# Kernel optimization log

Measured on AMD Instinct MI355X. Metric: run time of the kernel, lower is better.

Reference implementation:

```python
import jax, jax.numpy as jnp
import numpy as np

B, S, D, H = 2, 2048, 1024, 16
HD = D // H  # head size 64

def setup_inputs() -> dict:
    key = jax.random.key(0)
    ks = jax.random.split(key, 7)
    sc = 1.0 / np.sqrt(D)
    return {
        "batch_data": jax.random.normal(ks[0], (B, S, D), dtype=jnp.float32),
        "Wq": jax.random.normal(ks[1], (D, D), dtype=jnp.float32) * sc,
        "bq": jnp.zeros((D,), dtype=jnp.float32),
        "Wk": jax.random.normal(ks[2], (D, D), dtype=jnp.float32) * sc,
        "bk": jnp.zeros((D,), dtype=jnp.float32),
        "Wv": jax.random.normal(ks[3], (D, D), dtype=jnp.float32) * sc,
        "bv": jnp.zeros((D,), dtype=jnp.float32),
    }

def _split_heads(x):
    # [B,S,D] -> [B,H,S,HD]
    b, s, _ = x.shape
    return x.reshape(b, s, H, HD).transpose(0, 2, 1, 3)

def reference(batch_data, Wq, bq, Wk, bk, Wv, bv):
    q = _split_heads(batch_data @ Wq + bq)
    k = _split_heads(batch_data @ Wk + bk)
    v = _split_heads(batch_data @ Wv + bv)
    scores = jnp.einsum('bhqd,bhkd->bhqk', q, k) / jnp.sqrt(jnp.float32(HD))
    probs = jax.nn.softmax(scores, axis=-1)
    ctx = jnp.einsum('bhqk,bhkd->bhqd', probs, v)  # [B,H,S,HD]
    ctx = ctx.transpose(0, 2, 1, 3).reshape(batch_data.shape[0], batch_data.shape[1], D)
    return jnp.mean(ctx, axis=1)  # mean pool over sequence -> [B,D]
```

## Files before the change

### kernel.cpp

```cpp
#include <hip/hip_runtime.h>
#include <hip/hip_bf16.h>
#include <stdint.h>

#define B_  2
#define S_  2048
#define D_  1024
#define H_  16
#define HD_ 64

typedef __attribute__((ext_vector_type(8)))  __bf16 bf16x8;
typedef __attribute__((ext_vector_type(4)))  __bf16 bf16x4;
typedef __attribute__((ext_vector_type(2)))  __bf16 bf16x2;
typedef __attribute__((ext_vector_type(4)))  short  s16x4;
typedef __attribute__((ext_vector_type(4)))  float  f32x4;
typedef __attribute__((ext_vector_type(16))) float  f32x16;
typedef __attribute__((ext_vector_type(2)))  uint32_t u32x2;
typedef __attribute__((ext_vector_type(4)))  uint32_t u32x4;

#define QSCALE 0.18033688011112042f

#if __has_builtin(__builtin_amdgcn_mfma_f32_32x32x8bf16_1k)
#define HAVE_MFMA_K8 1
#else
#define HAVE_MFMA_K8 0
#endif

__device__ __forceinline__ void gload16(const void* g, void* l) {
  __builtin_amdgcn_global_load_lds(
      (__attribute__((address_space(1))) void*)(uintptr_t)g,
      (__attribute__((address_space(3))) void*)(uintptr_t)l,
      16, 0, 0);
}

__global__ __launch_bounds__(256) void prep(
    const float* __restrict__ x, const float* __restrict__ wq,
    const float* __restrict__ wk, const float* __restrict__ wv,
    __bf16* __restrict__ xb, __bf16* __restrict__ wt, float* __restrict__ out) {
  __shared__ float tile[32][33];
  const int t = threadIdx.x;
  const int bx = blockIdx.x;
  if (bx < 4096) {
    int i = bx * 256 + t;
    float4 v = ((const float4*)x)[i];
    bf16x4 o;
    o[0] = (__bf16)v.x; o[1] = (__bf16)v.y; o[2] = (__bf16)v.z; o[3] = (__bf16)v.w;
    ((bf16x4*)xb)[i] = o;
  } else if (bx < 7168) {
    int tb = bx - 4096;
    int z = tb >> 10;
    int rem = tb & 1023;
    int n0 = (rem & 31) * 32, k0 = (rem >> 5) * 32;
    const float* w = (z == 0) ? wq : (z == 1 ? wk : wv);
    __bf16* o = wt + (size_t)z * D_ * D_;
    int tx = t & 31, ty = t >> 5;
    for (int i = 0; i < 4; ++i)
      tile[ty + 8 * i][tx] = w[(size_t)(k0 + ty + 8 * i) * D_ + n0 + tx];
    __syncthreads();
    for (int i = 0; i < 4; ++i)
      o[(size_t)(n0 + ty + 8 * i) * D_ + k0 + tx] = (__bf16)tile[tx][ty + 8 * i];
  } else {
    float4* o4 = (float4*)out;
    float4 z4 = {0.f, 0.f, 0.f, 0.f};
    o4[t] = z4;
    o4[t + 256] = z4;
  }
}

__global__ __launch_bounds__(256, 3) void gemm_qkv(
    const __bf16* __restrict__ xb, const __bf16* __restrict__ wt,
    const float* __restrict__ bq, const float* __restrict__ bk,
    const float* __restrict__ bv, __bf16* __restrict__ qh,
    __bf16* __restrict__ kh, __bf16* __restrict__ vt) {
  constexpr int K = 1024;
  constexpr int NIT = K / 32;
  __shared__ __attribute__((aligned(16))) __bf16 lA[2][128 * 32];
  __shared__ __attribute__((aligned(16))) __bf16 lB[2][128 * 32];

  const int z = blockIdx.z;
  const __bf16* w = wt + (size_t)z * K * D_;
  const float* bias = (z == 0) ? bq : (z == 1 ? bk : bv);
  const int t = threadIdx.x;
  const int lane = t & 63;
  const int wid = t >> 6;
  const int quad = lane >> 4;
  const int col = lane & 15;
  const int m0 = blockIdx.x * 128;
  const int n0 = blockIdx.y * 128;
  const int wr = (wid >> 1) * 64;
  const int wc = (wid & 1) * 64;

  const int sr0 = t >> 2;
  const int gc = (t & 3) ^ ((t >> 2) & 3);

  auto stage = [&](int kt, int buf) {
    gload16(xb + (size_t)(m0 + sr0) * K + kt * 32 + gc * 8,
            (char*)&lA[buf][0] + t * 16);
    gload16(xb + (size_t)(m0 + 64 + sr0) * K + kt * 32 + gc * 8,
            (char*)&lA[buf][0] + 4096 + t * 16);
    gload16(w + (size_t)(n0 + sr0) * K + kt * 32 + gc * 8,
            (char*)&lB[buf][0] + t * 16);
    gload16(w + (size_t)(n0 + 64 + sr0) * K + kt * 32 + gc * 8,
            (char*)&lB[buf][0] + 4096 + t * 16);
  };

  f32x4 acc[4][4] = {};

  stage(0, 0);

  if (z < 2) {
    for (int kt = 0; kt < NIT; ++kt) {
      const int cur = kt & 1;
      __syncthreads();
      if (kt + 1 < NIT) stage(kt + 1, cur ^ 1);
      bf16x8 fw[4], fx[4];
      for (int i = 0; i < 4; ++i) {
        int n = wr + i * 16 + col;
        int sl = quad ^ (n & 3);
        fw[i] = *(const bf16x8*)((const char*)&lB[cur][0] + n * 64 + sl * 16);
      }
      for (int j = 0; j < 4; ++j) {
        int m = wc + j * 16 + col;
        int sl = quad ^ (m & 3);
        fx[j] = *(const bf16x8*)((const char*)&lA[cur][0] + m * 64 + sl * 16);
      }
      for (int i = 0; i < 4; ++i)
        for (int j = 0; j < 4; ++j)
          acc[i][j] = __builtin_amdgcn_mfma_f32_16x16x32_bf16(
              fw[i], fx[j], acc[i][j], 0, 0, 0);
    }
    const float scale = (z == 0) ? QSCALE : 1.0f;
    __bf16* dst = (z == 0) ? qh : kh;
    for (int i = 0; i < 4; ++i) {
      int gnb = n0 + wr + i * 16 + quad * 4;
      float4 bi = *(const float4*)(bias + gnb);
      int h = gnb >> 6, hd = gnb & 63;
      for (int j = 0; j < 4; ++j) {
        int gm = m0 + wc + j * 16 + col;
        int b = gm >> 11, s = gm & 2047;
        bf16x4 pk;
        pk[0] = (__bf16)((acc[i][j][0] + bi.x) * scale);
        pk[1] = (__bf16)((acc[i][j][1] + bi.y) * scale);
        pk[2] = (__bf16)((acc[i][j][2] + bi.z) * scale);
        pk[3] = (__bf16)((acc[i][j][3] + bi.w) * scale);
        *(bf16x4*)(dst + ((size_t)(b * H_ + h) * S_ + s) * HD_ + hd) = pk;
      }
    }
  } else {
    for (int kt = 0; kt < NIT; ++kt) {
      const int cur = kt & 1;
      __syncthreads();
      if (kt + 1 < NIT) stage(kt + 1, cur ^ 1);
      bf16x8 fx[4], fw[4];
      for (int i = 0; i < 4; ++i) {
        int m = wr + i * 16 + col;
        int sl = quad ^ (m & 3);
        fx[i] = *(const bf16x8*)((const char*)&lA[cur][0] + m * 64 + sl * 16);
      }
      for (int j = 0; j < 4; ++j) {
        int n = wc + j * 16 + col;
        int sl = quad ^ (n & 3);
        fw[j] = *(const bf16x8*)((const char*)&lB[cur][0] + n * 64 + sl * 16);
      }
      for (int i = 0; i < 4; ++i)
        for (int j = 0; j < 4; ++j)
          acc[i][j] = __builtin_amdgcn_mfma_f32_16x16x32_bf16(
              fx[i], fw[j], acc[i][j], 0, 0, 0);
    }
    for (int i = 0; i < 4; ++i) {
      int gmb = m0 + wr + i * 16 + quad * 4;
      int b = gmb >> 11, s = gmb & 2047;
      for (int j = 0; j < 4; ++j) {
        int gn = n0 + wc + j * 16 + col;
        int h = gn >> 6, hd = gn & 63;
        float bi = bias[gn];
        bf16x4 pk;
        pk[0] = (__bf16)(acc[i][j][0] + bi);
        pk[1] = (__bf16)(acc[i][j][1] + bi);
        pk[2] = (__bf16)(acc[i][j][2] + bi);
        pk[3] = (__bf16)(acc[i][j][3] + bi);
        *(bf16x4*)(vt + ((size_t)(b * H_ + h) * HD_ + hd) * S_ + s) = pk;
      }
    }
  }
}

__global__ __launch_bounds__(256, 4) void attn1(
    const __bf16* __restrict__ qh, const __bf16* __restrict__ kh,
    const __bf16* __restrict__ vt, __bf16* __restrict__ po,
    float* __restrict__ pl) {
  __shared__ __attribute__((aligned(16))) __bf16 lK[2][64 * 64];
  __shared__ __attribute__((aligned(16))) __bf16 lV[2][64 * 64];

  const int t = threadIdx.x;
  const int lane = t & 63;
  const int half = lane >> 5;
  const int q31 = lane & 31;
  const int bh = blockIdx.x;
  const int kc = blockIdx.z;
  const int q0w = blockIdx.y * 128 + (t >> 6) * 32;

  const __bf16* qbase = qh + (size_t)bh * S_ * HD_;
  const __bf16* kbase = kh + (size_t)bh * S_ * HD_;
  const __bf16* vbase = vt + (size_t)bh * HD_ * S_;

  bf16x8 aq[4];
  for (int ks = 0; ks < 4; ++ks)
    aq[ks] = *(const bf16x8*)(qbase + (size_t)(q0w + q31) * HD_ + ks * 16 + half * 8);

  f32x16 o[2] = {};
  float lsum = 0.f;

  const int srow = t >> 3;
  const int sgc = (t & 7) ^ (srow & 7);

  auto stage = [&](int kt, int buf) {
    gload16(kbase + (size_t)(kt * 64 + srow) * HD_ + sgc * 8,
            (char*)&lK[buf][0] + t * 16);
    gload16(kbase + (size_t)(kt * 64 + 32 + srow) * HD_ + sgc * 8,
            (char*)&lK[buf][0] + 4096 + t * 16);
    gload16(vbase + (size_t)srow * S_ + kt * 64 + sgc * 8,
            (char*)&lV[buf][0] + t * 16);
    gload16(vbase + (size_t)(32 + srow) * S_ + kt * 64 + sgc * 8,
            (char*)&lV[buf][0] + 4096 + t * 16);
  };

  stage(kc * 16, 0);

  for (int kt0 = 0; kt0 < 16; ++kt0) {
    const int cur = kt0 & 1;
    __syncthreads();
    if (kt0 + 1 < 16) stage(kc * 16 + kt0 + 1, cur ^ 1);

    for (int st = 0; st < 2; ++st) {
      f32x16 sc = {};
      const int row = st * 32 + q31;
      for (int ks = 0; ks < 4; ++ks) {
        int pos = (2 * ks + half) ^ (row & 7);
        bf16x8 fk = *(const bf16x8*)((const char*)&lK[cur][0] + row * 128 + pos * 16);
        sc = __builtin_amdgcn_mfma_f32_32x32x16_bf16(fk, aq[ks], sc, 0, 0, 0);
      }

      uint32_t pk[8];
      for (int p = 0; p < 8; ++p) {
        float ea = __builtin_amdgcn_exp2f(sc[2 * p]);
        float eb = __builtin_amdgcn_exp2f(sc[2 * p + 1]);
        lsum += ea;
        lsum += eb;
        uint32_t au = __builtin_bit_cast(uint32_t, ea) + 0x8000u;
        uint32_t bu = __builtin_bit_cast(uint32_t, eb) + 0x8000u;
        pk[p] = __builtin_amdgcn_perm(bu, au, 0x07060302u);
      }

#if HAVE_MFMA_K8
      for (int hdt = 0; hdt < 2; ++hdt) {
        const int rowv = hdt * 32 + q31;
        for (int g = 0; g < 4; ++g) {
          int pos = (4 * st + g) ^ (rowv & 7);
          s16x4 fv = *(const s16x4*)((const char*)&lV[cur][0] + rowv * 128 +
                                     pos * 16 + half * 8);
          u32x2 fpu = {pk[2 * g], pk[2 * g + 1]};
          s16x4 fp = __builtin_bit_cast(s16x4, fpu);
          o[hdt] = __builtin_amdgcn_mfma_f32_32x32x8bf16_1k(fv, fp, o[hdt], 0, 0, 0);
        }
      }
#else
      uint32_t x[8];
      for (int p = 0; p < 8; ++p) x[p] = __shfl_xor((int)pk[p], 32);
      bool h1 = (half != 0);
      u32x4 f0 = {h1 ? x[2] : pk[0], h1 ? x[3] : pk[1],
                  h1 ? pk[2] : x[0], h1 ? pk[3] : x[1]};
      u32x4 f1 = {h1 ? x[6] : pk[4], h1 ? x[7] : pk[5],
                  h1 ? pk[6] : x[4], h1 ? pk[7] : x[5]};
      bf16x8 Fa = __builtin_bit_cast(bf16x8, f0);
      bf16x8 Fb = __builtin_bit_cast(bf16x8, f1);
      for (int hdt = 0; hdt < 2; ++hdt) {
        const int rowv = hdt * 32 + q31;
        int ch0 = (4 * st + half) ^ (rowv & 7);
        int ch1 = (4 * st + 2 + half) ^ (rowv & 7);
        bf16x8 fv0 = *(const bf16x8*)((const char*)&lV[cur][0] + rowv * 128 + ch0 * 16);
        bf16x8 fv1 = *(const bf16x8*)((const char*)&lV[cur][0] + rowv * 128 + ch1 * 16);
        o[hdt] = __builtin_amdgcn_mfma_f32_32x32x16_bf16(fv0, Fa, o[hdt], 0, 0, 0);
        o[hdt] = __builtin_amdgcn_mfma_f32_32x32x16_bf16(fv1, Fb, o[hdt], 0, 0, 0);
      }
#endif
    }
  }

  float ltot = lsum + __shfl_xor(lsum, 32);
  const size_t slab = (size_t)(kc * 32 + bh) * S_;
  const int qrow = q0w + q31;
  if (half == 0) pl[slab + qrow] = ltot;
  for (int hdt = 0; hdt < 2; ++hdt)
    for (int rq = 0; rq < 4; ++rq) {
      bf16x4 pk;
      pk[0] = (__bf16)o[hdt][rq * 4 + 0];
      pk[1] = (__bf16)o[hdt][rq * 4 + 1];
      pk[2] = (__bf16)o[hdt][rq * 4 + 2];
      pk[3] = (__bf16)o[hdt][rq * 4 + 3];
      *(bf16x4*)(po + (slab + qrow) * HD_ + hdt * 32 + rq * 8 + half * 4) = pk;
    }
}

__global__ __launch_bounds__(256) void attn2(const __bf16* __restrict__ po,
                                             const float* __restrict__ pl,
                                             float* __restrict__ out) {
  __shared__ float red[256];
  const int t = threadIdx.x;
  const int hd = t & 63;
  const int rgrp = t >> 6;
  const int bh = blockIdx.y;
  const int r0 = blockIdx.x * 256 + rgrp * 64;
  const size_t s0 = (size_t)bh * S_;
  const size_t s1 = (size_t)(32 + bh) * S_;
  float acc = 0.f;
  for (int i = 0; i < 64; ++i) {
    int row = r0 + i;
    float l = pl[s0 + row] + pl[s1 + row];
    float v = (float)po[(s0 + row) * HD_ + hd] +
              (float)po[(s1 + row) * HD_ + hd];
    acc += v / l;
  }
  red[t] = acc;
  __syncthreads();
  if (t < 64) {
    float s = red[t] + red[t + 64] + red[t + 128] + red[t + 192];
    atomicAdd(out + (size_t)(bh >> 4) * D_ + (bh & 15) * HD_ + hd,
              s * (1.0f / S_));
  }
}

extern "C" void kernel_launch(void* const* d_in, const int* in_sizes, int n_in,
                              void* d_out, int out_size, void* d_ws, size_t ws_size,
                              hipStream_t stream) {
  const float* x  = (const float*)d_in[0];
  const float* Wq = (const float*)d_in[1];
  const float* bq = (const float*)d_in[2];
  const float* Wk = (const float*)d_in[3];
  const float* bk = (const float*)d_in[4];
  const float* Wv = (const float*)d_in[5];
  const float* bv = (const float*)d_in[6];
  float* out = (float*)d_out;

  char* ws = (char*)d_ws;
  __bf16* qh = (__bf16*)(ws);
  __bf16* kh = (__bf16*)(ws + ((size_t)8  << 20));
  __bf16* vt = (__bf16*)(ws + ((size_t)16 << 20));
  __bf16* xb = (__bf16*)(ws + ((size_t)24 << 20));
  __bf16* wt = (__bf16*)(ws + ((size_t)32 << 20));
  __bf16* po = (__bf16*)(ws + ((size_t)24 << 20));
  float*  pl = (float*) (ws + ((size_t)40 << 20));

  prep<<<dim3(7169), dim3(256), 0, stream>>>(x, Wq, Wk, Wv, xb, wt, out);
  gemm_qkv<<<dim3(32, 8, 3), dim3(256), 0, stream>>>(xb, wt, bq, bk, bv, qh, kh, vt);
  attn1<<<dim3(B_ * H_, S_ / 128, 2), dim3(256), 0, stream>>>(qh, kh, vt, po, pl);
  attn2<<<dim3(8, B_ * H_), dim3(256), 0, stream>>>(po, pl, out);
}
```

Measured before the change: 172.7 us.

## Shrink QKV GEMM tile to 128x64 and spread attn2 reduction over more blocks

```diff
diff --git a/kernel.cpp b/kernel.cpp
--- a/kernel.cpp
+++ b/kernel.cpp
@@ -11,19 +11,11 @@
 typedef __attribute__((ext_vector_type(8)))  __bf16 bf16x8;
 typedef __attribute__((ext_vector_type(4)))  __bf16 bf16x4;
 typedef __attribute__((ext_vector_type(2)))  __bf16 bf16x2;
-typedef __attribute__((ext_vector_type(4)))  short  s16x4;
 typedef __attribute__((ext_vector_type(4)))  float  f32x4;
 typedef __attribute__((ext_vector_type(16))) float  f32x16;
-typedef __attribute__((ext_vector_type(2)))  uint32_t u32x2;
 typedef __attribute__((ext_vector_type(4)))  uint32_t u32x4;
 
 #define QSCALE 0.18033688011112042f
-
-#if __has_builtin(__builtin_amdgcn_mfma_f32_32x32x8bf16_1k)
-#define HAVE_MFMA_K8 1
-#else
-#define HAVE_MFMA_K8 0
-#endif
 
 __device__ __forceinline__ void gload16(const void* g, void* l) {
   __builtin_amdgcn_global_load_lds(
@@ -66,7 +58,7 @@
   }
 }
 
-__global__ __launch_bounds__(256, 3) void gemm_qkv(
+__global__ __launch_bounds__(256, 4) void gemm_qkv(
     const __bf16* __restrict__ xb, const __bf16* __restrict__ wt,
     const float* __restrict__ bq, const float* __restrict__ bk,
     const float* __restrict__ bv, __bf16* __restrict__ qh,
@@ -74,7 +66,7 @@
   constexpr int K = 1024;
   constexpr int NIT = K / 32;
   __shared__ __attribute__((aligned(16))) __bf16 lA[2][128 * 32];
-  __shared__ __attribute__((aligned(16))) __bf16 lB[2][128 * 32];
+  __shared__ __attribute__((aligned(16))) __bf16 lB[2][64 * 32];
 
   const int z = blockIdx.z;
   const __bf16* w = wt + (size_t)z * K * D_;
@@ -85,9 +77,7 @@
   const int quad = lane >> 4;
   const int col = lane & 15;
   const int m0 = blockIdx.x * 128;
-  const int n0 = blockIdx.y * 128;
-  const int wr = (wid >> 1) * 64;
-  const int wc = (wid & 1) * 64;
+  const int n0 = blockIdx.y * 64;
 
   const int sr0 = t >> 2;
   const int gc = (t & 3) ^ ((t >> 2) & 3);
@@ -99,11 +89,9 @@
             (char*)&lA[buf][0] + 4096 + t * 16);
     gload16(w + (size_t)(n0 + sr0) * K + kt * 32 + gc * 8,
             (char*)&lB[buf][0] + t * 16);
-    gload16(w + (size_t)(n0 + 64 + sr0) * K + kt * 32 + gc * 8,
-            (char*)&lB[buf][0] + 4096 + t * 16);
   };
 
-  f32x4 acc[4][4] = {};
+  f32x4 acc[4][2] = {};
 
   stage(0, 0);
 
@@ -112,30 +100,30 @@
       const int cur = kt & 1;
       __syncthreads();
       if (kt + 1 < NIT) stage(kt + 1, cur ^ 1);
-      bf16x8 fw[4], fx[4];
+      bf16x8 fw[4], fx[2];
       for (int i = 0; i < 4; ++i) {
-        int n = wr + i * 16 + col;
+        int n = i * 16 + col;
         int sl = quad ^ (n & 3);
         fw[i] = *(const bf16x8*)((const char*)&lB[cur][0] + n * 64 + sl * 16);
       }
-      for (int j = 0; j < 4; ++j) {
-        int m = wc + j * 16 + col;
+      for (int j = 0; j < 2; ++j) {
+        int m = wid * 32 + j * 16 + col;
         int sl = quad ^ (m & 3);
         fx[j] = *(const bf16x8*)((const char*)&lA[cur][0] + m * 64 + sl * 16);
       }
       for (int i = 0; i < 4; ++i)
-        for (int j = 0; j < 4; ++j)
+        for (int j = 0; j < 2; ++j)
           acc[i][j] = __builtin_amdgcn_mfma_f32_16x16x32_bf16(
               fw[i], fx[j], acc[i][j], 0, 0, 0);
     }
     const float scale = (z == 0) ? QSCALE : 1.0f;
     __bf16* dst = (z == 0) ? qh : kh;
     for (int i = 0; i < 4; ++i) {
-      int gnb = n0 + wr + i * 16 + quad * 4;
+      int gnb = n0 + i * 16 + quad * 4;
       float4 bi = *(const float4*)(bias + gnb);
       int h = gnb >> 6, hd = gnb & 63;
-      for (int j = 0; j < 4; ++j) {
-        int gm = m0 + wc + j * 16 + col;
+      for (int j = 0; j < 2; ++j) {
+        int gm = m0 + wid * 32 + j * 16 + col;
         int b = gm >> 11, s = gm & 2047;
         bf16x4 pk;
         pk[0] = (__bf16)((acc[i][j][0] + bi.x) * scale);
@@ -150,34 +138,34 @@
       const int cur = kt & 1;
       __syncthreads();
       if (kt + 1 < NIT) stage(kt + 1, cur ^ 1);
-      bf16x8 fx[4], fw[4];
-      for (int i = 0; i < 4; ++i) {
-        int m = wr + i * 16 + col;
+      bf16x8 fx[2], fw[4];
+      for (int i = 0; i < 2; ++i) {
+        int m = wid * 32 + i * 16 + col;
         int sl = quad ^ (m & 3);
         fx[i] = *(const bf16x8*)((const char*)&lA[cur][0] + m * 64 + sl * 16);
       }
       for (int j = 0; j < 4; ++j) {
-        int n = wc + j * 16 + col;
+        int n = j * 16 + col;
         int sl = quad ^ (n & 3);
         fw[j] = *(const bf16x8*)((const char*)&lB[cur][0] + n * 64 + sl * 16);
       }
-      for (int i = 0; i < 4; ++i)
-        for (int j = 0; j < 4; ++j)
-          acc[i][j] = __builtin_amdgcn_mfma_f32_16x16x32_bf16(
-              fx[i], fw[j], acc[i][j], 0, 0, 0);
-    }
-    for (int i = 0; i < 4; ++i) {
-      int gmb = m0 + wr + i * 16 + quad * 4;
+      for (int j = 0; j < 4; ++j)
+        for (int i = 0; i < 2; ++i)
+          acc[j][i] = __builtin_amdgcn_mfma_f32_16x16x32_bf16(
+              fx[i], fw[j], acc[j][i], 0, 0, 0);
+    }
+    for (int i = 0; i < 2; ++i) {
+      int gmb = m0 + wid * 32 + i * 16 + quad * 4;
       int b = gmb >> 11, s = gmb & 2047;
       for (int j = 0; j < 4; ++j) {
-        int gn = n0 + wc + j * 16 + col;
+        int gn = n0 + j * 16 + col;
         int h = gn >> 6, hd = gn & 63;
         float bi = bias[gn];
         bf16x4 pk;
-        pk[0] = (__bf16)(acc[i][j][0] + bi);
-        pk[1] = (__bf16)(acc[i][j][1] + bi);
-        pk[2] = (__bf16)(acc[i][j][2] + bi);
-        pk[3] = (__bf16)(acc[i][j][3] + bi);
+        pk[0] = (__bf16)(acc[j][i][0] + bi);
+        pk[1] = (__bf16)(acc[j][i][1] + bi);
+        pk[2] = (__bf16)(acc[j][i][2] + bi);
+        pk[3] = (__bf16)(acc[j][i][3] + bi);
         *(bf16x4*)(vt + ((size_t)(b * H_ + h) * HD_ + hd) * S_ + s) = pk;
       }
     }
@@ -251,19 +239,6 @@
         pk[p] = __builtin_amdgcn_perm(bu, au, 0x07060302u);
       }
 
-#if HAVE_MFMA_K8
-      for (int hdt = 0; hdt < 2; ++hdt) {
-        const int rowv = hdt * 32 + q31;
-        for (int g = 0; g < 4; ++g) {
-          int pos = (4 * st + g) ^ (rowv & 7);
-          s16x4 fv = *(const s16x4*)((const char*)&lV[cur][0] + rowv * 128 +
-                                     pos * 16 + half * 8);
-          u32x2 fpu = {pk[2 * g], pk[2 * g + 1]};
-          s16x4 fp = __builtin_bit_cast(s16x4, fpu);
-          o[hdt] = __builtin_amdgcn_mfma_f32_32x32x8bf16_1k(fv, fp, o[hdt], 0, 0, 0);
-        }
-      }
-#else
       uint32_t x[8];
       for (int p = 0; p < 8; ++p) x[p] = __shfl_xor((int)pk[p], 32);
       bool h1 = (half != 0);
@@ -273,6 +248,7 @@
                   h1 ? pk[6] : x[4], h1 ? pk[7] : x[5]};
       bf16x8 Fa = __builtin_bit_cast(bf16x8, f0);
       bf16x8 Fb = __builtin_bit_cast(bf16x8, f1);
+
       for (int hdt = 0; hdt < 2; ++hdt) {
         const int rowv = hdt * 32 + q31;
         int ch0 = (4 * st + half) ^ (rowv & 7);
@@ -282,7 +258,6 @@
         o[hdt] = __builtin_amdgcn_mfma_f32_32x32x16_bf16(fv0, Fa, o[hdt], 0, 0, 0);
         o[hdt] = __builtin_amdgcn_mfma_f32_32x32x16_bf16(fv1, Fb, o[hdt], 0, 0, 0);
       }
-#endif
     }
   }
 
@@ -309,11 +284,12 @@
   const int hd = t & 63;
   const int rgrp = t >> 6;
   const int bh = blockIdx.y;
-  const int r0 = blockIdx.x * 256 + rgrp * 64;
+  const int r0 = blockIdx.x * 64 + rgrp * 16;
   const size_t s0 = (size_t)bh * S_;
   const size_t s1 = (size_t)(32 + bh) * S_;
   float acc = 0.f;
-  for (int i = 0; i < 64; ++i) {
+#pragma unroll 4
+  for (int i = 0; i < 16; ++i) {
     int row = r0 + i;
     float l = pl[s0 + row] + pl[s1 + row];
     float v = (float)po[(s0 + row) * HD_ + hd] +
@@ -351,7 +327,7 @@
   float*  pl = (float*) (ws + ((size_t)40 << 20));
 
   prep<<<dim3(7169), dim3(256), 0, stream>>>(x, Wq, Wk, Wv, xb, wt, out);
-  gemm_qkv<<<dim3(32, 8, 3), dim3(256), 0, stream>>>(xb, wt, bq, bk, bv, qh, kh, vt);
+  gemm_qkv<<<dim3(32, 16, 3), dim3(256), 0, stream>>>(xb, wt, bq, bk, bv, qh, kh, vt);
   attn1<<<dim3(B_ * H_, S_ / 128, 2), dim3(256), 0, stream>>>(qh, kh, vt, po, pl);
-  attn2<<<dim3(8, B_ * H_), dim3(256), 0, stream>>>(po, pl, out);
-}
+  attn2<<<dim3(32, B_ * H_), dim3(256), 0, stream>>>(po, pl, out);
+}
```

Measured after the change: 177.4 us. 1.03x slower.

## Process two query tiles per wave in attention to reuse K/V LDS fragments

Applied to the files above, without the earlier changes.

```diff
diff --git a/kernel.cpp b/kernel.cpp
--- a/kernel.cpp
+++ b/kernel.cpp
@@ -15,15 +15,8 @@
 typedef __attribute__((ext_vector_type(4)))  float  f32x4;
 typedef __attribute__((ext_vector_type(16))) float  f32x16;
 typedef __attribute__((ext_vector_type(2)))  uint32_t u32x2;
-typedef __attribute__((ext_vector_type(4)))  uint32_t u32x4;
 
 #define QSCALE 0.18033688011112042f
-
-#if __has_builtin(__builtin_amdgcn_mfma_f32_32x32x8bf16_1k)
-#define HAVE_MFMA_K8 1
-#else
-#define HAVE_MFMA_K8 0
-#endif
 
 __device__ __forceinline__ void gload16(const void* g, void* l) {
   __builtin_amdgcn_global_load_lds(
@@ -184,7 +177,7 @@
   }
 }
 
-__global__ __launch_bounds__(256, 4) void attn1(
+__global__ __launch_bounds__(256, 2) void attn1(
     const __bf16* __restrict__ qh, const __bf16* __restrict__ kh,
     const __bf16* __restrict__ vt, __bf16* __restrict__ po,
     float* __restrict__ pl) {
@@ -197,18 +190,20 @@
   const int q31 = lane & 31;
   const int bh = blockIdx.x;
   const int kc = blockIdx.z;
-  const int q0w = blockIdx.y * 128 + (t >> 6) * 32;
+  const int q0w = blockIdx.y * 256 + (t >> 6) * 64;
 
   const __bf16* qbase = qh + (size_t)bh * S_ * HD_;
   const __bf16* kbase = kh + (size_t)bh * S_ * HD_;
   const __bf16* vbase = vt + (size_t)bh * HD_ * S_;
 
-  bf16x8 aq[4];
-  for (int ks = 0; ks < 4; ++ks)
-    aq[ks] = *(const bf16x8*)(qbase + (size_t)(q0w + q31) * HD_ + ks * 16 + half * 8);
-
-  f32x16 o[2] = {};
-  float lsum = 0.f;
+  bf16x8 aq[2][4];
+  for (int qt = 0; qt < 2; ++qt)
+    for (int ks = 0; ks < 4; ++ks)
+      aq[qt][ks] = *(const bf16x8*)(qbase +
+          (size_t)(q0w + qt * 32 + q31) * HD_ + ks * 16 + half * 8);
+
+  f32x16 o[2][2] = {};
+  float lsum[2] = {0.f, 0.f};
 
   const int srow = t >> 3;
   const int sgc = (t & 7) ^ (srow & 7);
@@ -232,73 +227,67 @@
     if (kt0 + 1 < 16) stage(kc * 16 + kt0 + 1, cur ^ 1);
 
     for (int st = 0; st < 2; ++st) {
-      f32x16 sc = {};
+      f32x16 sc0 = {}, sc1 = {};
       const int row = st * 32 + q31;
       for (int ks = 0; ks < 4; ++ks) {
         int pos = (2 * ks + half) ^ (row & 7);
         bf16x8 fk = *(const bf16x8*)((const char*)&lK[cur][0] + row * 128 + pos * 16);
-        sc = __builtin_amdgcn_mfma_f32_32x32x16_bf16(fk, aq[ks], sc, 0, 0, 0);
-      }
-
-      uint32_t pk[8];
+        sc0 = __builtin_amdgcn_mfma_f32_32x32x16_bf16(fk, aq[0][ks], sc0, 0, 0, 0);
+        sc1 = __builtin_amdgcn_mfma_f32_32x32x16_bf16(fk, aq[1][ks], sc1, 0, 0, 0);
+      }
+
+      uint32_t pk0[8], pk1[8];
       for (int p = 0; p < 8; ++p) {
-        float ea = __builtin_amdgcn_exp2f(sc[2 * p]);
-        float eb = __builtin_amdgcn_exp2f(sc[2 * p + 1]);
-        lsum += ea;
-        lsum += eb;
+        float ea = __builtin_amdgcn_exp2f(sc0[2 * p]);
+        float eb = __builtin_amdgcn_exp2f(sc0[2 * p + 1]);
+        lsum[0] += ea;
+        lsum[0] += eb;
         uint32_t au = __builtin_bit_cast(uint32_t, ea) + 0x8000u;
         uint32_t bu = __builtin_bit_cast(uint32_t, eb) + 0x8000u;
-        pk[p] = __builtin_amdgcn_perm(bu, au, 0x07060302u);
-      }
-
-#if HAVE_MFMA_K8
+        pk0[p] = __builtin_amdgcn_perm(bu, au, 0x07060302u);
+      }
+      for (int p = 0; p < 8; ++p) {
+        float ea = __builtin_amdgcn_exp2f(sc1[2 * p]);
+        float eb = __builtin_amdgcn_exp2f(sc1[2 * p + 1]);
+        lsum[1] += ea;
+        lsum[1] += eb;
+        uint32_t au = __builtin_bit_cast(uint32_t, ea) + 0x8000u;
+        uint32_t bu = __builtin_bit_cast(uint32_t, eb) + 0x8000u;
+        pk1[p] = __builtin_amdgcn_perm(bu, au, 0x07060302u);
+      }
+
       for (int hdt = 0; hdt < 2; ++hdt) {
         const int rowv = hdt * 32 + q31;
         for (int g = 0; g < 4; ++g) {
           int pos = (4 * st + g) ^ (rowv & 7);
           s16x4 fv = *(const s16x4*)((const char*)&lV[cur][0] + rowv * 128 +
                                      pos * 16 + half * 8);
-          u32x2 fpu = {pk[2 * g], pk[2 * g + 1]};
-          s16x4 fp = __builtin_bit_cast(s16x4, fpu);
-          o[hdt] = __builtin_amdgcn_mfma_f32_32x32x8bf16_1k(fv, fp, o[hdt], 0, 0, 0);
+          u32x2 fp0u = {pk0[2 * g], pk0[2 * g + 1]};
+          u32x2 fp1u = {pk1[2 * g], pk1[2 * g + 1]};
+          o[0][hdt] = __builtin_amdgcn_mfma_f32_32x32x8bf16_1k(
+              fv, __builtin_bit_cast(s16x4, fp0u), o[0][hdt], 0, 0, 0);
+          o[1][hdt] = __builtin_amdgcn_mfma_f32_32x32x8bf16_1k(
+              fv, __builtin_bit_cast(s16x4, fp1u), o[1][hdt], 0, 0, 0);
         }
       }
-#else
-      uint32_t x[8];
-      for (int p = 0; p < 8; ++p) x[p] = __shfl_xor((int)pk[p], 32);
-      bool h1 = (half != 0);
-      u32x4 f0 = {h1 ? x[2] : pk[0], h1 ? x[3] : pk[1],
-                  h1 ? pk[2] : x[0], h1 ? pk[3] : x[1]};
-      u32x4 f1 = {h1 ? x[6] : pk[4], h1 ? x[7] : pk[5],
-                  h1 ? pk[6] : x[4], h1 ? pk[7] : x[5]};
-      bf16x8 Fa = __builtin_bit_cast(bf16x8, f0);
-      bf16x8 Fb = __builtin_bit_cast(bf16x8, f1);
-      for (int hdt = 0; hdt < 2; ++hdt) {
-        const int rowv = hdt * 32 + q31;
-        int ch0 = (4 * st + half) ^ (rowv & 7);
-        int ch1 = (4 * st + 2 + half) ^ (rowv & 7);
-        bf16x8 fv0 = *(const bf16x8*)((const char*)&lV[cur][0] + rowv * 128 + ch0 * 16);
-        bf16x8 fv1 = *(const bf16x8*)((const char*)&lV[cur][0] + rowv * 128 + ch1 * 16);
-        o[hdt] = __builtin_amdgcn_mfma_f32_32x32x16_bf16(fv0, Fa, o[hdt], 0, 0, 0);
-        o[hdt] = __builtin_amdgcn_mfma_f32_32x32x16_bf16(fv1, Fb, o[hdt], 0, 0, 0);
-      }
-#endif
-    }
-  }
-
-  float ltot = lsum + __shfl_xor(lsum, 32);
+    }
+  }
+
   const size_t slab = (size_t)(kc * 32 + bh) * S_;
-  const int qrow = q0w + q31;
-  if (half == 0) pl[slab + qrow] = ltot;
-  for (int hdt = 0; hdt < 2; ++hdt)
-    for (int rq = 0; rq < 4; ++rq) {
-      bf16x4 pk;
-      pk[0] = (__bf16)o[hdt][rq * 4 + 0];
-      pk[1] = (__bf16)o[hdt][rq * 4 + 1];
-      pk[2] = (__bf16)o[hdt][rq * 4 + 2];
-      pk[3] = (__bf16)o[hdt][rq * 4 + 3];
-      *(bf16x4*)(po + (slab + qrow) * HD_ + hdt * 32 + rq * 8 + half * 4) = pk;
-    }
+  for (int qt = 0; qt < 2; ++qt) {
+    float ltot = lsum[qt] + __shfl_xor(lsum[qt], 32);
+    const int qrow = q0w + qt * 32 + q31;
+    if (half == 0) pl[slab + qrow] = ltot;
+    for (int hdt = 0; hdt < 2; ++hdt)
+      for (int rq = 0; rq < 4; ++rq) {
+        bf16x4 pk;
+        pk[0] = (__bf16)o[qt][hdt][rq * 4 + 0];
+        pk[1] = (__bf16)o[qt][hdt][rq * 4 + 1];
+        pk[2] = (__bf16)o[qt][hdt][rq * 4 + 2];
+        pk[3] = (__bf16)o[qt][hdt][rq * 4 + 3];
+        *(bf16x4*)(po + (slab + qrow) * HD_ + hdt * 32 + rq * 8 + half * 4) = pk;
+      }
+  }
 }
 
 __global__ __launch_bounds__(256) void attn2(const __bf16* __restrict__ po,
@@ -309,11 +298,12 @@
   const int hd = t & 63;
   const int rgrp = t >> 6;
   const int bh = blockIdx.y;
-  const int r0 = blockIdx.x * 256 + rgrp * 64;
+  const int r0 = blockIdx.x * 64 + rgrp * 16;
   const size_t s0 = (size_t)bh * S_;
   const size_t s1 = (size_t)(32 + bh) * S_;
   float acc = 0.f;
-  for (int i = 0; i < 64; ++i) {
+#pragma unroll 4
+  for (int i = 0; i < 16; ++i) {
     int row = r0 + i;
     float l = pl[s0 + row] + pl[s1 + row];
     float v = (float)po[(s0 + row) * HD_ + hd] +
@@ -352,6 +342,6 @@
 
   prep<<<dim3(7169), dim3(256), 0, stream>>>(x, Wq, Wk, Wv, xb, wt, out);
   gemm_qkv<<<dim3(32, 8, 3), dim3(256), 0, stream>>>(xb, wt, bq, bk, bv, qh, kh, vt);
-  attn1<<<dim3(B_ * H_, S_ / 128, 2), dim3(256), 0, stream>>>(qh, kh, vt, po, pl);
-  attn2<<<dim3(8, B_ * H_), dim3(256), 0, stream>>>(po, pl, out);
-}
+  attn1<<<dim3(B_ * H_, 8, 2), dim3(256), 0, stream>>>(qh, kh, vt, po, pl);
+  attn2<<<dim3(32, B_ * H_), dim3(256), 0, stream>>>(po, pl, out);
+}
```

Result: faster. 163.2 us (-5.5%).
